# Performance work log

Hardware: AMD Instinct MI355X
Metric: run time of the kernel (lower is better)

The kernel has to match this reference:

```python
import jax, jax.numpy as jnp
import numpy as np

C = 16; HIDDEN = 64; FIRE_RATE = 0.5; ADV_DT = 0.25; ADV_STEPS = 2
DIFF_RATE = 0.05; V_NOISE = 0.2; V_DAMP = 0.95
MASS, VX, VY = 3, 4, 5


def _nb(s, a, b):
    # value at (y+a, x+b) with circular (torus) padding
    return jnp.roll(s, (-a, -b), axis=(1, 2))


def perceive(s):
    # Multi-scale NCA perception: identity + sobel_x + sobel_y + laplacian, circular padding.
    gx = (_nb(s, -1, 1) + 2.0 * _nb(s, 0, 1) + _nb(s, 1, 1)
          - _nb(s, -1, -1) - 2.0 * _nb(s, 0, -1) - _nb(s, 1, -1)) / 8.0
    gy = (_nb(s, 1, -1) + 2.0 * _nb(s, 1, 0) + _nb(s, 1, 1)
          - _nb(s, -1, -1) - 2.0 * _nb(s, -1, 0) - _nb(s, -1, 1)) / 8.0
    lap = (_nb(s, 0, 1) + _nb(s, 0, -1) + _nb(s, 1, 0) + _nb(s, -1, 0) - 4.0 * s) / 4.0
    return jnp.concatenate([s, gx, gy, lap], axis=-1)  # (B,H,W,4C)


def advect_mass(mass, vx, vy, dt):
    # Semi-Lagrangian backward trace with periodic bilinear sampling. mass: (B,H,W)
    B, H, W = mass.shape
    yy, xx = jnp.meshgrid(jnp.arange(H, dtype=mass.dtype), jnp.arange(W, dtype=mass.dtype), indexing='ij')
    sy = yy[None] - vy * dt
    sx = xx[None] - vx * dt
    y0f = jnp.floor(sy); x0f = jnp.floor(sx)
    fy = sy - y0f; fx = sx - x0f
    y0 = jnp.mod(y0f.astype(jnp.int32), H); y1 = jnp.mod(y0 + 1, H)
    x0 = jnp.mod(x0f.astype(jnp.int32), W); x1 = jnp.mod(x0 + 1, W)
    b = jnp.arange(B)[:, None, None]
    m00 = mass[b, y0, x0]; m01 = mass[b, y0, x1]
    m10 = mass[b, y1, x0]; m11 = mass[b, y1, x1]
    return (1.0 - fy) * ((1.0 - fx) * m00 + fx * m01) + fy * ((1.0 - fx) * m10 + fx * m11)


def diffuse_mass(mass, rate):
    m = mass[..., None]
    avg4 = (_nb(m, 0, 1) + _nb(m, 0, -1) + _nb(m, 1, 0) + _nb(m, -1, 0))[..., 0] / 4.0
    return mass + rate * (avg4 - mass)


def setup_inputs() -> dict:
    key = jax.random.key(0)
    ks = jax.random.split(key, 12)
    B, H, W = 8, 512, 512
    P = 4 * C  # perception channels
    state = jax.random.normal(ks[0], (B, H, W, C), dtype=jnp.float32)
    # 1x1 conv kernels stored as (Cin, Cout). Zero-init heads replaced by small
    # random values so the full pipeline (advection included) is exercised.
    s = 0.1
    return {
        'state': state,
        'seed': 0,
        'w1': jax.random.normal(ks[1], (P, HIDDEN), jnp.float32) * s,
        'b1': jnp.zeros((HIDDEN,), jnp.float32),
        'w2': jax.random.normal(ks[2], (HIDDEN, HIDDEN // 2), jnp.float32) * s,
        'b2': jnp.zeros((HIDDEN // 2,), jnp.float32),
        'w_rgb': jax.random.normal(ks[3], (HIDDEN // 2, 3), jnp.float32) * s,
        'b_rgb': jnp.zeros((3,), jnp.float32),
        'w_vel': jax.random.normal(ks[4], (HIDDEN // 2, 2), jnp.float32) * s,
        'b_vel': jnp.zeros((2,), jnp.float32),
        'w_hid': jax.random.normal(ks[5], (HIDDEN // 2, 8), jnp.float32) * s,
        'b_hid': jnp.zeros((8,), jnp.float32),
    }


def reference(state, seed, w1, b1, w2, b2, w_rgb, b_rgb, w_vel, b_vel, w_hid, b_hid):
    key = jax.random.key(seed)
    p = perceive(state)  # (B,H,W,64)
    x = jax.nn.relu(jnp.einsum('bhwc,cd->bhwd', p, w1) + b1)
    x = jax.nn.relu(jnp.einsum('bhwc,cd->bhwd', x, w2) + b2)
    rgb = jnp.einsum('bhwc,cd->bhwd', x, w_rgb) + b_rgb
    vel = jnp.einsum('bhwc,cd->bhwd', x, w_vel) + b_vel
    hid = jnp.einsum('bhwc,cd->bhwd', x, w_hid) + b_hid
    z1 = jnp.zeros(x.shape[:-1] + (1,), x.dtype)  # mass update forced to 0
    z2 = jnp.zeros(x.shape[:-1] + (2,), x.dtype)  # target velocity update 0
    ds = jnp.concatenate([rgb, z1, vel, z2, hid], axis=-1)  # (B,H,W,16)
    # stochastic per-cell update
    mask = jax.random.bernoulli(key, FIRE_RATE, state.shape[:-1] + (1,)).astype(state.dtype)
    state = state + ds * mask
    # clip + damp velocity
    state = state.at[..., VX].set(jnp.clip(state[..., VX], -1.0, 1.0))
    state = state.at[..., VY].set(jnp.clip(state[..., VY], -1.0, 1.0))
    vx = V_DAMP * state[..., VX]
    vy = V_DAMP * state[..., VY]
    state = state.at[..., VX].set(vx).at[..., VY].set(vy)
    # velocity noise (transport only, not written back)
    key, nk = jax.random.split(key)
    k1, k2 = jax.random.split(nk)
    vx = vx + V_NOISE * jax.random.normal(k1, vx.shape, vx.dtype)
    vy = vy + V_NOISE * jax.random.normal(k2, vy.shape, vy.dtype)
    mass = state[..., MASS]
    for _ in range(ADV_STEPS):
        mass = advect_mass(mass, vx, vy, ADV_DT)
    mass = diffuse_mass(mass, DIFF_RATE)
    state = state.at[..., MASS].set(mass)
    state = state.at[..., :3].set(jnp.clip(state[..., :3], 0.0, 1.0))
    return state
```

## Files before the change

### kernel.cpp

```cpp
#include <hip/hip_runtime.h>
#include <hip/hip_fp16.h>

#define HH 512
#define WW 512
#define NB 8
#define TS 16
#define LROW 19
#define LPLANE (18*LROW)
#define PROW 68

typedef unsigned int u32;
typedef __attribute__((ext_vector_type(4))) _Float16 f16x4;
typedef __attribute__((ext_vector_type(8))) _Float16 f16x8;
typedef __attribute__((ext_vector_type(4))) float f32x4;

__device__ __forceinline__ u32 rotl32(u32 v, int n){ return (v<<n)|(v>>(32-n)); }
struct U2 { u32 x, y; };

__device__ __forceinline__ U2 threefry2x32(u32 k0, u32 k1, u32 x0, u32 x1){
  u32 k2 = k0 ^ k1 ^ 0x1BD11BDAu;
  x0 += k0; x1 += k1;
  const int RA[4] = {13,15,26,6};
  const int RB[4] = {17,29,16,24};
  #pragma unroll
  for(int i=0;i<4;i++){ x0+=x1; x1=rotl32(x1,RA[i]); x1^=x0; }
  x0 += k1; x1 += k2 + 1u;
  #pragma unroll
  for(int i=0;i<4;i++){ x0+=x1; x1=rotl32(x1,RB[i]); x1^=x0; }
  x0 += k2; x1 += k0 + 2u;
  #pragma unroll
  for(int i=0;i<4;i++){ x0+=x1; x1=rotl32(x1,RA[i]); x1^=x0; }
  x0 += k0; x1 += k1 + 3u;
  #pragma unroll
  for(int i=0;i<4;i++){ x0+=x1; x1=rotl32(x1,RB[i]); x1^=x0; }
  x0 += k1; x1 += k2 + 4u;
  #pragma unroll
  for(int i=0;i<4;i++){ x0+=x1; x1=rotl32(x1,RA[i]); x1^=x0; }
  x0 += k2; x1 += k0 + 5u;
  U2 r; r.x = x0; r.y = x1; return r;
}

__device__ __forceinline__ u32 pbits(u32 k0, u32 k1, u32 i){
  U2 o = threefry2x32(k0, k1, 0u, i);
  return o.x ^ o.y;
}

__device__ __forceinline__ float xla_erfinv(float x){
  float w = -log1pf(-x*x);
  float p;
  if (w < 5.0f){
    w -= 2.5f;
    p = 2.81022636e-08f;
    p = fmaf(p,w, 3.43273939e-07f);
    p = fmaf(p,w,-3.5233877e-06f);
    p = fmaf(p,w,-4.39150654e-06f);
    p = fmaf(p,w, 0.00021858087f);
    p = fmaf(p,w,-0.00125372503f);
    p = fmaf(p,w,-0.00417768164f);
    p = fmaf(p,w, 0.246640727f);
    p = fmaf(p,w, 1.50140941f);
  } else {
    w = sqrtf(w) - 3.0f;
    p = -0.000200214257f;
    p = fmaf(p,w, 0.000100950558f);
    p = fmaf(p,w, 0.00134934322f);
    p = fmaf(p,w,-0.00367342844f);
    p = fmaf(p,w, 0.00573950773f);
    p = fmaf(p,w,-0.0076224613f);
    p = fmaf(p,w, 0.00943887047f);
    p = fmaf(p,w, 1.00167406f);
    p = fmaf(p,w, 2.83297682f);
  }
  return p*x;
}

__device__ __forceinline__ float normal_from_bits(u32 bits){
  const float LO = -0.99999994f;
  u32 fb = (bits >> 9) | 0x3F800000u;
  float f = __uint_as_float(fb) - 1.0f;
  float u = f * 2.0f + LO;
  u = fmaxf(LO, u);
  return 1.41421356f * xla_erfinv(u);
}

__device__ __forceinline__ void noise_keys(int seed, u32& k1a, u32& k1b, u32& k2a, u32& k2b){
  u32 K0 = 0u, K1 = (u32)seed;
  U2 nk = threefry2x32(K0, K1, 0u, 1u);
  U2 c1 = threefry2x32(nk.x, nk.y, 0u, 0u);
  U2 c2 = threefry2x32(nk.x, nk.y, 0u, 1u);
  k1a = c1.x; k1b = c1.y;
  k2a = c2.x; k2b = c2.y;
}

__device__ __forceinline__ u32 h2_as_u32(__half2 h){ return *(u32*)&h; }
__device__ __forceinline__ __half2 u32_as_h2(u32 v){ return *(__half2*)&v; }

__global__ void prep_w(const float* __restrict__ w1, const float* __restrict__ w2,
                       const float* __restrict__ wrgb, const float* __restrict__ wvel,
                       const float* __restrict__ whid,
                       const float* __restrict__ brgb, const float* __restrict__ bvel,
                       const float* __restrict__ bhid,
                       unsigned short* __restrict__ wfrag, float* __restrict__ bcat){
  int tid = threadIdx.x;
  for (int f = tid >> 6; f < 13; f += 4){
    int lane = tid & 63, quad = lane >> 4, m = lane & 15;
    #pragma unroll
    for (int j = 0; j < 8; ++j){
      float val;
      if (f < 8){
        int kh = f >> 2, nc = f & 3;
        int k = kh*32 + quad*8 + j, n = nc*16 + m;
        val = w1[k*64 + n];
      } else if (f < 12){
        int g = f - 8, kh = g >> 1, nc = g & 1;
        int k = kh*32 + quad*8 + j, n = nc*16 + m;
        val = w2[k*32 + n];
      } else {
        int k = quad*8 + j;
        val = (m < 3) ? wrgb[k*3 + m]
            : (m == 4 || m == 5) ? wvel[k*2 + (m-4)]
            : (m >= 8) ? whid[k*8 + (m-8)] : 0.0f;
      }
      wfrag[(f*64 + lane)*8 + j] = __half_as_ushort(__float2half(val));
    }
  }
  if (tid < 16)
    bcat[tid] = (tid < 3) ? brgb[tid]
              : (tid == 4 || tid == 5) ? bvel[tid-4]
              : (tid >= 8) ? bhid[tid-8] : 0.0f;
}

__global__ __launch_bounds__(256, 4) void nca_main(
    const float* __restrict__ st, const int* __restrict__ seedp,
    const float* __restrict__ b1, const float* __restrict__ b2,
    const unsigned short* __restrict__ wfrag, const float* __restrict__ bcat,
    float* __restrict__ out, u32* __restrict__ vxy, float* __restrict__ m0p)
{
  __shared__ __align__(16) unsigned char smem[256*PROW*2];
  u32 (*ls2)[LPLANE] = (u32 (*)[LPLANE])smem;
  unsigned short* pbuf = (unsigned short*)smem;

  const int tid  = threadIdx.x;
  const int lane = tid & 63, wv = tid >> 6;
  const int quad = lane >> 4, mm = lane & 15;
  const int bx = blockIdx.x, by = blockIdx.y, b = blockIdx.z;
  const int x0t = bx*TS, y0t = by*TS;
  const float* __restrict__ sb = st + (size_t)b*HH*WW*16;

  f16x8 Bf[13];
  #pragma unroll
  for (int f = 0; f < 13; ++f)
    Bf[f] = *(const f16x8*)(wfrag + (f*64 + lane)*8);
  float bias1[4], bias2[2];
  #pragma unroll
  for (int nc = 0; nc < 4; ++nc) bias1[nc] = b1[nc*16 + mm];
  #pragma unroll
  for (int nc = 0; nc < 2; ++nc) bias2[nc] = b2[nc*16 + mm];
  float biasH = bcat[mm];

  for (int t = tid; t < 18*18*4; t += 256){
    int pix = t >> 2, part = t & 3;
    int py = pix / 18, px = pix - py*18;
    int gy = (y0t + py - 1) & (HH-1);
    int gx = (x0t + px - 1) & (WW-1);
    const float4 v = *(const float4*)(sb + ((gy*WW + gx)*16 + part*4));
    int li = py*LROW + px;
    ls2[part*2  ][li] = h2_as_u32(__floats2half2_rn(v.x, v.y));
    ls2[part*2+1][li] = h2_as_u32(__floats2half2_rn(v.z, v.w));
  }
  __syncthreads();

  const int lx = tid & 15, ly = tid >> 4;
  const int ctr = (ly+1)*LROW + (lx+1);

  const __half2 two    = __float2half2_rn(2.0f);
  const __half2 eighth = __float2half2_rn(0.125f);
  const __half2 quart  = __float2half2_rn(0.25f);
  const __half2 neg4   = __float2half2_rn(-4.0f);
  u32 rid[8], rgx[8], rgy[8], rlp[8];
  #pragma unroll
  for (int cp = 0; cp < 8; ++cp){
    const u32* pl = ls2[cp];
    __half2 t00 = u32_as_h2(pl[ctr-LROW-1]), t01 = u32_as_h2(pl[ctr-LROW]), t02 = u32_as_h2(pl[ctr-LROW+1]);
    __half2 t10 = u32_as_h2(pl[ctr-1]),      t11 = u32_as_h2(pl[ctr]),      t12 = u32_as_h2(pl[ctr+1]);
    __half2 t20 = u32_as_h2(pl[ctr+LROW-1]), t21 = u32_as_h2(pl[ctr+LROW]), t22 = u32_as_h2(pl[ctr+LROW+1]);
    __half2 sR = __hfma2(two, t12, __hadd2(t02, t22));
    __half2 sL = __hfma2(two, t10, __hadd2(t00, t20));
    __half2 sB = __hfma2(two, t21, __hadd2(t20, t22));
    __half2 sT = __hfma2(two, t01, __hadd2(t00, t02));
    __half2 sC = __hadd2(__hadd2(t10, t12), __hadd2(t01, t21));
    rid[cp] = h2_as_u32(t11);
    rgx[cp] = h2_as_u32(__hmul2(__hsub2(sR, sL), eighth));
    rgy[cp] = h2_as_u32(__hmul2(__hsub2(sB, sT), eighth));
    rlp[cp] = h2_as_u32(__hmul2(__hfma2(neg4, t11, sC), quart));
  }
  __syncthreads();

  {
    u32* pb32 = (u32*)pbuf;
    #pragma unroll
    for (int cp = 0; cp < 8; ++cp){
      pb32[tid*34 +      cp] = rid[cp];
      pb32[tid*34 +  8 + cp] = rgx[cp];
      pb32[tid*34 + 16 + cp] = rgy[cp];
      pb32[tid*34 + 24 + cp] = rlp[cp];
    }
  }

  const int rowbase = wv*4;
  const _Float16* pb16 = (const _Float16*)pbuf;

  auto loadfrag = [&](int px, int choff) -> f16x8 {
    const _Float16* ar = pb16 + px*PROW + choff;
    f16x4 lo = *(const f16x4*)ar;
    f16x4 hi = *(const f16x4*)(ar + 4);
    return __builtin_shufflevector(lo, hi, 0,1,2,3,4,5,6,7);
  };

  f32x4 C1[4][4];
  #pragma unroll
  for (int gi = 0; gi < 4; ++gi){
    int px = (rowbase+gi)*16 + mm;
    f16x8 a0 = loadfrag(px, quad*8);
    f16x8 a1 = loadfrag(px, 32 + quad*8);
    #pragma unroll
    for (int nc = 0; nc < 4; ++nc){
      f32x4 c; c[0]=bias1[nc]; c[1]=bias1[nc]; c[2]=bias1[nc]; c[3]=bias1[nc];
      c = __builtin_amdgcn_mfma_f32_16x16x32_f16(a0, Bf[nc],   c, 0,0,0);
      c = __builtin_amdgcn_mfma_f32_16x16x32_f16(a1, Bf[4+nc], c, 0,0,0);
      C1[gi][nc] = c;
    }
  }
  #pragma unroll
  for (int gi = 0; gi < 4; ++gi)
    #pragma unroll
    for (int nc = 0; nc < 4; ++nc)
      #pragma unroll
      for (int r = 0; r < 4; ++r)
        pbuf[((rowbase+gi)*16 + quad*4 + r)*PROW + nc*16 + mm] =
            __half_as_ushort(__float2half(fmaxf(C1[gi][nc][r], 0.0f)));

  f32x4 C2[4][2];
  #pragma unroll
  for (int gi = 0; gi < 4; ++gi){
    int px = (rowbase+gi)*16 + mm;
    f16x8 a0 = loadfrag(px, quad*8);
    f16x8 a1 = loadfrag(px, 32 + quad*8);
    #pragma unroll
    for (int nc = 0; nc < 2; ++nc){
      f32x4 c; c[0]=bias2[nc]; c[1]=bias2[nc]; c[2]=bias2[nc]; c[3]=bias2[nc];
      c = __builtin_amdgcn_mfma_f32_16x16x32_f16(a0, Bf[8+nc],  c, 0,0,0);
      c = __builtin_amdgcn_mfma_f32_16x16x32_f16(a1, Bf[10+nc], c, 0,0,0);
      C2[gi][nc] = c;
    }
  }
  #pragma unroll
  for (int gi = 0; gi < 4; ++gi)
    #pragma unroll
    for (int nc = 0; nc < 2; ++nc)
      #pragma unroll
      for (int r = 0; r < 4; ++r)
        pbuf[((rowbase+gi)*16 + quad*4 + r)*PROW + nc*16 + mm] =
            __half_as_ushort(__float2half(fmaxf(C2[gi][nc][r], 0.0f)));

  f32x4 C3[4];
  #pragma unroll
  for (int gi = 0; gi < 4; ++gi){
    int px = (rowbase+gi)*16 + mm;
    f16x8 a0 = loadfrag(px, quad*8);
    f32x4 c; c[0]=biasH; c[1]=biasH; c[2]=biasH; c[3]=biasH;
    C3[gi] = __builtin_amdgcn_mfma_f32_16x16x32_f16(a0, Bf[12], c, 0,0,0);
  }
  __syncthreads();
  {
    float* dsb = (float*)smem;
    #pragma unroll
    for (int gi = 0; gi < 4; ++gi)
      #pragma unroll
      for (int r = 0; r < 4; ++r)
        dsb[((rowbase+gi)*16 + quad*4 + r)*17 + mm] = C3[gi][r];
  }

  const float* dsb = (const float*)smem;
  int seed = seedp[0];
  u32 K0 = 0u, K1 = (u32)seed;
  const int ygl = y0t + ly, xgl = x0t + lx;
  const u32 pix = ((u32)b*HH + ygl)*WW + xgl;
  u32 mbits = pbits(K0, K1, pix);
  float m = ((int)mbits >= 0) ? 1.0f : 0.0f;

  const float* scp = sb + ((size_t)(ygl*WW + xgl))*16;
  float4 s0 = *(const float4*)(scp+0),  s1 = *(const float4*)(scp+4);
  float4 s2 = *(const float4*)(scp+8),  s3 = *(const float4*)(scp+12);
  float sc[16] = {s0.x,s0.y,s0.z,s0.w, s1.x,s1.y,s1.z,s1.w,
                  s2.x,s2.y,s2.z,s2.w, s3.x,s3.y,s3.z,s3.w};
  float ds[16], ns[16];
  #pragma unroll
  for (int ch = 0; ch < 16; ++ch) ds[ch] = dsb[tid*17 + ch];
  ds[3] = 0.0f; ds[6] = 0.0f; ds[7] = 0.0f;
  #pragma unroll
  for (int ch = 0; ch < 16; ++ch) ns[ch] = sc[ch] + ds[ch]*m;

  ns[4] = 0.95f * fminf(fmaxf(ns[4], -1.0f), 1.0f);
  ns[5] = 0.95f * fminf(fmaxf(ns[5], -1.0f), 1.0f);
  ns[0] = fminf(fmaxf(ns[0], 0.0f), 1.0f);
  ns[1] = fminf(fmaxf(ns[1], 0.0f), 1.0f);
  ns[2] = fminf(fmaxf(ns[2], 0.0f), 1.0f);
  ns[3] = sc[3];

  float* __restrict__ op = out + (size_t)pix*16;
  *(float4*)(op+ 0) = make_float4(ns[0],ns[1],ns[2],ns[3]);
  *(float4*)(op+ 4) = make_float4(ns[4],ns[5],ns[6],ns[7]);
  *(float4*)(op+ 8) = make_float4(ns[8],ns[9],ns[10],ns[11]);
  *(float4*)(op+12) = make_float4(ns[12],ns[13],ns[14],ns[15]);

  u32 k1a,k1b,k2a,k2b; noise_keys(seed, k1a,k1b,k2a,k2b);
  float vx = ns[4] + 0.2f*normal_from_bits(pbits(k1a,k1b,pix));
  float vy = ns[5] + 0.2f*normal_from_bits(pbits(k2a,k2b,pix));
  vxy[pix] = h2_as_u32(__floats2half2_rn(vx, vy));
  m0p[pix] = sc[3];
}

#define AT 32
__global__ __launch_bounds__(256) void advect_fused(
    const float* __restrict__ m0, const u32* __restrict__ vxy,
    float* __restrict__ out)
{
  __shared__ float sm0[38][39];
  __shared__ u32   sv [36][37];
  __shared__ float sm1[36][37];
  __shared__ float sm2[34][35];
  const int tid = threadIdx.x;
  const int X0 = blockIdx.x*AT, Y0 = blockIdx.y*AT, b = blockIdx.z;
  const size_t base = ((size_t)b) << 18;

  for (int t = tid; t < 38*38; t += 256){
    int ly = t/38, lx = t - ly*38;
    int gy = (Y0-3+ly)&511, gx = (X0-3+lx)&511;
    sm0[ly][lx] = m0[base + (gy<<9) + gx];
  }
  for (int t = tid; t < 36*36; t += 256){
    int ly = t/36, lx = t - ly*36;
    int gy = (Y0-2+ly)&511, gx = (X0-2+lx)&511;
    sv[ly][lx] = vxy[base + (gy<<9) + gx];
  }
  __syncthreads();

  for (int t = tid; t < 36*36; t += 256){
    int ly = t/36, lx = t - ly*36;
    int gy = (Y0-2+ly)&511, gx = (X0-2+lx)&511;
    __half2 hv = u32_as_h2(sv[ly][lx]);
    float vx = __low2float(hv), vyv = __high2float(hv);
    float sy = (float)gy - vyv*0.25f;
    float sx = (float)gx - vx *0.25f;
    float y0f = floorf(sy), x0f = floorf(sx);
    float fy = sy - y0f, fx = sx - x0f;
    int l0y = (((int)y0f) - Y0 + 3) & 511;
    int l0x = (((int)x0f) - X0 + 3) & 511;
    float m00 = sm0[l0y][l0x],   m01 = sm0[l0y][l0x+1];
    float m10 = sm0[l0y+1][l0x], m11 = sm0[l0y+1][l0x+1];
    sm1[ly][lx] = (1.0f-fy)*((1.0f-fx)*m00 + fx*m01) + fy*((1.0f-fx)*m10 + fx*m11);
  }
  __syncthreads();

  for (int t = tid; t < 34*34; t += 256){
    int ly = t/34, lx = t - ly*34;
    int gy = (Y0-1+ly)&511, gx = (X0-1+lx)&511;
    __half2 hv = u32_as_h2(sv[ly+1][lx+1]);
    float vx = __low2float(hv), vyv = __high2float(hv);
    float sy = (float)gy - vyv*0.25f;
    float sx = (float)gx - vx *0.25f;
    float y0f = floorf(sy), x0f = floorf(sx);
    float fy = sy - y0f, fx = sx - x0f;
    int l0y = (((int)y0f) - Y0 + 2) & 511;
    int l0x = (((int)x0f) - X0 + 2) & 511;
    float m00 = sm1[l0y][l0x],   m01 = sm1[l0y][l0x+1];
    float m10 = sm1[l0y+1][l0x], m11 = sm1[l0y+1][l0x+1];
    sm2[ly][lx] = (1.0f-fy)*((1.0f-fx)*m00 + fx*m01) + fy*((1.0f-fx)*m10 + fx*m11);
  }
  __syncthreads();

  for (int t = tid; t < 32*32; t += 256){
    int ly = t >> 5, lx = t & 31;
    int gy = Y0 + ly, gx = X0 + lx;
    float c = sm2[ly+1][lx+1];
    float r = sm2[ly+1][lx+2], l = sm2[ly+1][lx];
    float d = sm2[ly+2][lx+1], u = sm2[ly][lx+1];
    out[(base + (gy<<9) + gx)*16 + 3] = c + 0.05f*((r+l+d+u)*0.25f - c);
  }
}

extern "C" void kernel_launch(void* const* d_in, const int* in_sizes, int n_in,
                              void* d_out, int out_size, void* d_ws, size_t ws_size,
                              hipStream_t stream)
{
  const float* st   = (const float*)d_in[0];
  const int*   seed = (const int*)  d_in[1];
  const float* w1   = (const float*)d_in[2];
  const float* b1   = (const float*)d_in[3];
  const float* w2   = (const float*)d_in[4];
  const float* b2   = (const float*)d_in[5];
  const float* wrgb = (const float*)d_in[6];
  const float* brgb = (const float*)d_in[7];
  const float* wvel = (const float*)d_in[8];
  const float* bvel = (const float*)d_in[9];
  const float* whid = (const float*)d_in[10];
  const float* bhid = (const float*)d_in[11];
  float* out = (float*)d_out;

  const int npix = NB*HH*WW;
  float* m0p = (float*)d_ws;
  u32*   vxy = (u32*)(m0p + npix);
  unsigned short* wfrag = (unsigned short*)(vxy + npix);
  float* bcat = (float*)(wfrag + 13*64*8);

  prep_w<<<1, 256, 0, stream>>>(w1, w2, wrgb, wvel, whid, brgb, bvel, bhid, wfrag, bcat);

  dim3 gridA(WW/TS, HH/TS, NB);
  nca_main<<<gridA, 256, 0, stream>>>(st, seed, b1, b2, wfrag, bcat, out, vxy, m0p);

  dim3 gridB(WW/AT, HH/AT, NB);
  advect_fused<<<gridB, 256, 0, stream>>>(m0p, vxy, out);
}
```

Measured before the change: 414.2 us.

## Swizzle LDS perception buffer, split weight fragments, precompute noise keys to raise occupancy

Replaces the padded 68-half row layout of the perception/hidden buffer with a 64-half row using an XOR swizzle, so fragments load as single 16-byte reads and LDS shrinks to 32 KB. Weight fragments are split into two register groups loaded only where needed, and GEMM outputs are stored per row-group instead of held in registers. Launch bounds rise from 4 to 5 blocks per CU. Noise threefry keys are computed once in prep_w instead of per thread. The intent is lower register and LDS pressure for higher occupancy and fewer LDS bank conflicts, at the risk of spills or swizzle indexing mistakes.

```diff
diff --git a/kernel.cpp b/kernel.cpp
--- a/kernel.cpp
+++ b/kernel.cpp
@@ -7,7 +7,7 @@
 #define TS 16
 #define LROW 19
 #define LPLANE (18*LROW)
-#define PROW 68
+#define SW(row) (((row) >> 1) & 7)
 
 typedef unsigned int u32;
 typedef __attribute__((ext_vector_type(4))) _Float16 f16x4;
@@ -83,15 +83,6 @@
   return 1.41421356f * xla_erfinv(u);
 }
 
-__device__ __forceinline__ void noise_keys(int seed, u32& k1a, u32& k1b, u32& k2a, u32& k2b){
-  u32 K0 = 0u, K1 = (u32)seed;
-  U2 nk = threefry2x32(K0, K1, 0u, 1u);
-  U2 c1 = threefry2x32(nk.x, nk.y, 0u, 0u);
-  U2 c2 = threefry2x32(nk.x, nk.y, 0u, 1u);
-  k1a = c1.x; k1b = c1.y;
-  k2a = c2.x; k2b = c2.y;
-}
-
 __device__ __forceinline__ u32 h2_as_u32(__half2 h){ return *(u32*)&h; }
 __device__ __forceinline__ __half2 u32_as_h2(u32 v){ return *(__half2*)&v; }
 
@@ -100,7 +91,9 @@
                        const float* __restrict__ whid,
                        const float* __restrict__ brgb, const float* __restrict__ bvel,
                        const float* __restrict__ bhid,
-                       unsigned short* __restrict__ wfrag, float* __restrict__ bcat){
+                       const int* __restrict__ seedp,
+                       unsigned short* __restrict__ wfrag, float* __restrict__ bcat,
+                       u32* __restrict__ nkeys){
   int tid = threadIdx.x;
   for (int f = tid >> 6; f < 13; f += 4){
     int lane = tid & 63, quad = lane >> 4, m = lane & 15;
@@ -128,17 +121,24 @@
     bcat[tid] = (tid < 3) ? brgb[tid]
               : (tid == 4 || tid == 5) ? bvel[tid-4]
               : (tid >= 8) ? bhid[tid-8] : 0.0f;
-}
-
-__global__ __launch_bounds__(256, 4) void nca_main(
+  if (tid == 0){
+    u32 K1 = (u32)seedp[0];
+    U2 nk = threefry2x32(0u, K1, 0u, 1u);
+    U2 c1 = threefry2x32(nk.x, nk.y, 0u, 0u);
+    U2 c2 = threefry2x32(nk.x, nk.y, 0u, 1u);
+    nkeys[0] = c1.x; nkeys[1] = c1.y; nkeys[2] = c2.x; nkeys[3] = c2.y;
+  }
+}
+
+__global__ __launch_bounds__(256, 5) void nca_main(
     const float* __restrict__ st, const int* __restrict__ seedp,
     const float* __restrict__ b1, const float* __restrict__ b2,
     const unsigned short* __restrict__ wfrag, const float* __restrict__ bcat,
+    const u32* __restrict__ nkeys,
     float* __restrict__ out, u32* __restrict__ vxy, float* __restrict__ m0p)
 {
-  __shared__ __align__(16) unsigned char smem[256*PROW*2];
+  __shared__ __align__(16) unsigned char smem[32768];
   u32 (*ls2)[LPLANE] = (u32 (*)[LPLANE])smem;
-  unsigned short* pbuf = (unsigned short*)smem;
 
   const int tid  = threadIdx.x;
   const int lane = tid & 63, wv = tid >> 6;
@@ -147,16 +147,18 @@
   const int x0t = bx*TS, y0t = by*TS;
   const float* __restrict__ sb = st + (size_t)b*HH*WW*16;
 
-  f16x8 Bf[13];
-  #pragma unroll
-  for (int f = 0; f < 13; ++f)
-    Bf[f] = *(const f16x8*)(wfrag + (f*64 + lane)*8);
+  f16x8 BfA[8];
+  #pragma unroll
+  for (int f = 0; f < 8; ++f)
+    BfA[f] = *(const f16x8*)(wfrag + (f*64 + lane)*8);
   float bias1[4], bias2[2];
   #pragma unroll
   for (int nc = 0; nc < 4; ++nc) bias1[nc] = b1[nc*16 + mm];
   #pragma unroll
   for (int nc = 0; nc < 2; ++nc) bias2[nc] = b2[nc*16 + mm];
   float biasH = bcat[mm];
+  const int seed = seedp[0];
+  const u32 k1a = nkeys[0], k1b = nkeys[1], k2a = nkeys[2], k2b = nkeys[3];
 
   for (int t = tid; t < 18*18*4; t += 256){
     int pix = t >> 2, part = t & 3;
@@ -197,79 +199,87 @@
   __syncthreads();
 
   {
-    u32* pb32 = (u32*)pbuf;
+    u32* pb32 = (u32*)smem;
+    const int rsw = SW(tid) << 2;
     #pragma unroll
     for (int cp = 0; cp < 8; ++cp){
-      pb32[tid*34 +      cp] = rid[cp];
-      pb32[tid*34 +  8 + cp] = rgx[cp];
-      pb32[tid*34 + 16 + cp] = rgy[cp];
-      pb32[tid*34 + 24 + cp] = rlp[cp];
+      pb32[tid*32 + (( 0 + cp) ^ rsw)] = rid[cp];
+      pb32[tid*32 + (( 8 + cp) ^ rsw)] = rgx[cp];
+      pb32[tid*32 + ((16 + cp) ^ rsw)] = rgy[cp];
+      pb32[tid*32 + ((24 + cp) ^ rsw)] = rlp[cp];
     }
   }
 
   const int rowbase = wv*4;
-  const _Float16* pb16 = (const _Float16*)pbuf;
-
-  auto loadfrag = [&](int px, int choff) -> f16x8 {
-    const _Float16* ar = pb16 + px*PROW + choff;
-    f16x4 lo = *(const f16x4*)ar;
-    f16x4 hi = *(const f16x4*)(ar + 4);
-    return __builtin_shufflevector(lo, hi, 0,1,2,3,4,5,6,7);
+  const _Float16* pb16 = (const _Float16*)smem;
+  unsigned short* pbuf = (unsigned short*)smem;
+
+  auto loadfrag = [&](int px, int chunk) -> f16x8 {
+    return *(const f16x8*)(pb16 + px*64 + ((chunk ^ SW(px)) * 8));
   };
 
-  f32x4 C1[4][4];
   #pragma unroll
   for (int gi = 0; gi < 4; ++gi){
     int px = (rowbase+gi)*16 + mm;
-    f16x8 a0 = loadfrag(px, quad*8);
-    f16x8 a1 = loadfrag(px, 32 + quad*8);
+    f16x8 a0 = loadfrag(px, quad);
+    f16x8 a1 = loadfrag(px, 4 + quad);
+    f32x4 C[4];
     #pragma unroll
     for (int nc = 0; nc < 4; ++nc){
       f32x4 c; c[0]=bias1[nc]; c[1]=bias1[nc]; c[2]=bias1[nc]; c[3]=bias1[nc];
-      c = __builtin_amdgcn_mfma_f32_16x16x32_f16(a0, Bf[nc],   c, 0,0,0);
-      c = __builtin_amdgcn_mfma_f32_16x16x32_f16(a1, Bf[4+nc], c, 0,0,0);
-      C1[gi][nc] = c;
+      c = __builtin_amdgcn_mfma_f32_16x16x32_f16(a0, BfA[nc],   c, 0,0,0);
+      c = __builtin_amdgcn_mfma_f32_16x16x32_f16(a1, BfA[4+nc], c, 0,0,0);
+      C[nc] = c;
     }
-  }
-  #pragma unroll
-  for (int gi = 0; gi < 4; ++gi)
     #pragma unroll
     for (int nc = 0; nc < 4; ++nc)
       #pragma unroll
-      for (int r = 0; r < 4; ++r)
-        pbuf[((rowbase+gi)*16 + quad*4 + r)*PROW + nc*16 + mm] =
-            __half_as_ushort(__float2half(fmaxf(C1[gi][nc][r], 0.0f)));
-
-  f32x4 C2[4][2];
+      for (int r = 0; r < 4; ++r){
+        int row = (rowbase+gi)*16 + quad*4 + r;
+        pbuf[row*64 + ((nc*16 + mm) ^ (SW(row) << 3))] =
+            __half_as_ushort(__float2half(fmaxf(C[nc][r], 0.0f)));
+      }
+  }
+
+  f16x8 BfB[5];
+  #pragma unroll
+  for (int f = 0; f < 5; ++f)
+    BfB[f] = *(const f16x8*)(wfrag + ((8+f)*64 + lane)*8);
+  const int ygl = y0t + ly, xgl = x0t + lx;
+  const float* scp = sb + ((size_t)(ygl*WW + xgl))*16;
+  float4 s0 = *(const float4*)(scp+0),  s1 = *(const float4*)(scp+4);
+  float4 s2 = *(const float4*)(scp+8),  s3 = *(const float4*)(scp+12);
+
   #pragma unroll
   for (int gi = 0; gi < 4; ++gi){
     int px = (rowbase+gi)*16 + mm;
-    f16x8 a0 = loadfrag(px, quad*8);
-    f16x8 a1 = loadfrag(px, 32 + quad*8);
+    f16x8 a0 = loadfrag(px, quad);
+    f16x8 a1 = loadfrag(px, 4 + quad);
+    f32x4 C[2];
     #pragma unroll
     for (int nc = 0; nc < 2; ++nc){
       f32x4 c; c[0]=bias2[nc]; c[1]=bias2[nc]; c[2]=bias2[nc]; c[3]=bias2[nc];
-      c = __builtin_amdgcn_mfma_f32_16x16x32_f16(a0, Bf[8+nc],  c, 0,0,0);
-      c = __builtin_amdgcn_mfma_f32_16x16x32_f16(a1, Bf[10+nc], c, 0,0,0);
-      C2[gi][nc] = c;
+      c = __builtin_amdgcn_mfma_f32_16x16x32_f16(a0, BfB[nc],   c, 0,0,0);
+      c = __builtin_amdgcn_mfma_f32_16x16x32_f16(a1, BfB[2+nc], c, 0,0,0);
+      C[nc] = c;
     }
-  }
-  #pragma unroll
-  for (int gi = 0; gi < 4; ++gi)
     #pragma unroll
     for (int nc = 0; nc < 2; ++nc)
       #pragma unroll
-      for (int r = 0; r < 4; ++r)
-        pbuf[((rowbase+gi)*16 + quad*4 + r)*PROW + nc*16 + mm] =
-            __half_as_ushort(__float2half(fmaxf(C2[gi][nc][r], 0.0f)));
+      for (int r = 0; r < 4; ++r){
+        int row = (rowbase+gi)*16 + quad*4 + r;
+        pbuf[row*64 + ((nc*16 + mm) ^ (SW(row) << 3))] =
+            __half_as_ushort(__float2half(fmaxf(C[nc][r], 0.0f)));
+      }
+  }
 
   f32x4 C3[4];
   #pragma unroll
   for (int gi = 0; gi < 4; ++gi){
     int px = (rowbase+gi)*16 + mm;
-    f16x8 a0 = loadfrag(px, quad*8);
+    f16x8 a0 = loadfrag(px, quad);
     f32x4 c; c[0]=biasH; c[1]=biasH; c[2]=biasH; c[3]=biasH;
-    C3[gi] = __builtin_amdgcn_mfma_f32_16x16x32_f16(a0, Bf[12], c, 0,0,0);
+    C3[gi] = __builtin_amdgcn_mfma_f32_16x16x32_f16(a0, BfB[4], c, 0,0,0);
   }
   __syncthreads();
   {
@@ -282,16 +292,11 @@
   }
 
   const float* dsb = (const float*)smem;
-  int seed = seedp[0];
   u32 K0 = 0u, K1 = (u32)seed;
-  const int ygl = y0t + ly, xgl = x0t + lx;
   const u32 pix = ((u32)b*HH + ygl)*WW + xgl;
   u32 mbits = pbits(K0, K1, pix);
   float m = ((int)mbits >= 0) ? 1.0f : 0.0f;
 
-  const float* scp = sb + ((size_t)(ygl*WW + xgl))*16;
-  float4 s0 = *(const float4*)(scp+0),  s1 = *(const float4*)(scp+4);
-  float4 s2 = *(const float4*)(scp+8),  s3 = *(const float4*)(scp+12);
   float sc[16] = {s0.x,s0.y,s0.z,s0.w, s1.x,s1.y,s1.z,s1.w,
                   s2.x,s2.y,s2.z,s2.w, s3.x,s3.y,s3.z,s3.w};
   float ds[16], ns[16];
@@ -314,7 +319,6 @@
   *(float4*)(op+ 8) = make_float4(ns[8],ns[9],ns[10],ns[11]);
   *(float4*)(op+12) = make_float4(ns[12],ns[13],ns[14],ns[15]);
 
-  u32 k1a,k1b,k2a,k2b; noise_keys(seed, k1a,k1b,k2a,k2b);
   float vx = ns[4] + 0.2f*normal_from_bits(pbits(k1a,k1b,pix));
   float vy = ns[5] + 0.2f*normal_from_bits(pbits(k2a,k2b,pix));
   vxy[pix] = h2_as_u32(__floats2half2_rn(vx, vy));
@@ -413,11 +417,13 @@
   u32*   vxy = (u32*)(m0p + npix);
   unsigned short* wfrag = (unsigned short*)(vxy + npix);
   float* bcat = (float*)(wfrag + 13*64*8);
-
-  prep_w<<<1, 256, 0, stream>>>(w1, w2, wrgb, wvel, whid, brgb, bvel, bhid, wfrag, bcat);
+  u32* nkeys = (u32*)(bcat + 16);
+
+  prep_w<<<1, 256, 0, stream>>>(w1, w2, wrgb, wvel, whid, brgb, bvel, bhid, seed,
+                                wfrag, bcat, nkeys);
 
   dim3 gridA(WW/TS, HH/TS, NB);
-  nca_main<<<gridA, 256, 0, stream>>>(st, seed, b1, b2, wfrag, bcat, out, vxy, m0p);
+  nca_main<<<gridA, 256, 0, stream>>>(st, seed, b1, b2, wfrag, bcat, nkeys, out, vxy, m0p);
 
   dim3 gridB(WW/AT, HH/AT, NB);
   advect_fused<<<gridB, 256, 0, stream>>>(m0p, vxy, out);
```

Measured after the change: 496.3 us. +19.8%, slower.
